# Optimization experiments

Hardware: AMD Instinct MI355X
Metric: run time of the kernel (lower is better)

Reference implementation:

```python
import jax, jax.numpy as jnp
import numpy as np
from jax import lax

TAU = 0.1
TAU_BASE = 0.1
DIR_W = 1.0
N_LEVELS = 3  # labels has N_LEVELS hierarchy cols + 1 direction col
B, D = 4096, 1024


def setup_inputs() -> dict:
    key = jax.random.key(0)
    k1, k2 = jax.random.split(key)
    embeddings = jax.random.normal(k1, (B, D), dtype=jnp.float32)
    labels = jax.random.randint(k2, (B, N_LEVELS + 1), 0, 8, dtype=jnp.int64)
    return {"embeddings": embeddings, "labels": labels}


def _hier_loss(embeddings, labels):
    # F.normalize(dim=1) with eps=1e-12
    norm = jnp.linalg.norm(embeddings, axis=1, keepdims=True)
    z = embeddings / jnp.maximum(norm, 1e-12)
    hier = labels[:, :-1]          # [B, n_levels]
    dirs = labels[:, -1]           # [B]
    n_levels = hier.shape[1]
    b = z.shape[0]
    eye = jnp.eye(b, dtype=bool)

    sim = (z @ z.T) / TAU                                   # [B, B]
    sim = sim - lax.stop_gradient(jnp.max(sim, axis=1, keepdims=True))
    diff_dir = (dirs[:, None] != dirs[None, :])
    sim = sim - DIR_W * diff_dir.astype(sim.dtype)
    sim = jnp.where(eye, -jnp.inf, sim)
    tiny = jnp.finfo(sim.dtype).tiny
    log_prob = sim - jnp.log(jnp.maximum(jnp.exp(sim).sum(axis=1, keepdims=True), tiny))

    same_dir = ~diff_dir
    total = jnp.zeros((), dtype=sim.dtype)
    max_lower = jnp.full((), -jnp.inf, dtype=sim.dtype)
    seen = jnp.zeros((), dtype=jnp.int32)

    for lvl in range(1, n_levels + 1):  # small fixed loop over hierarchy levels
        same_up_to = jnp.all(hier[:, None, :lvl] == hier[None, :, :lvl], axis=2)  # [B, B]
        pos_mask = same_up_to & same_dir & ~eye
        pos_counts = pos_mask.sum(axis=1)                   # [B] int
        valid = pos_counts > 0
        num_valid = valid.sum()
        any_valid = num_valid > 0

        masked_logp = jnp.where(pos_mask, log_prob, 0.0)
        per_row = masked_logp.sum(axis=1) / jnp.maximum(pos_counts, 1).astype(sim.dtype)
        mean_logp_pos = jnp.sum(jnp.where(valid, per_row, 0.0)) / jnp.maximum(num_valid, 1).astype(sim.dtype)
        raw_loss = -(TAU / TAU_BASE) * mean_logp_pos

        # hmce: running max over levels (max_lower is detached)
        level_loss = jnp.maximum(max_lower, raw_loss)
        max_lower = jnp.where(any_valid,
                              lax.stop_gradient(jnp.maximum(max_lower, level_loss)),
                              max_lower)
        penalty = 2.0 ** (1.0 / lvl)  # h_penalty(1/lvl)
        total = total + jnp.where(any_valid, level_loss * penalty, 0.0)
        seen = seen + any_valid.astype(jnp.int32)

    return total / jnp.maximum(seen, 1).astype(total.dtype)


def reference(embeddings, labels):
    return _hier_loss(embeddings, labels)
```

## Files before the change

kernel.cpp:

```cpp
#include <hip/hip_runtime.h>
#include <hip/hip_bf16.h>
#include <stdint.h>

#define NB 4096
#define ND 1024

typedef __attribute__((ext_vector_type(4))) float f32x4;
typedef __attribute__((ext_vector_type(2))) long i64x2;

__global__ __launch_bounds__(256) void prep_kernel(
    const float* __restrict__ emb, const int* __restrict__ labels,
    unsigned char* __restrict__ zq, int* __restrict__ keys)
{
    const int wid = threadIdx.x >> 6, lane = threadIdx.x & 63;
    const int row = blockIdx.x * 4 + wid;
    const float4* src = (const float4*)(emb + (size_t)row * ND) + lane * 4;
    float4 v[4];
    float ss = 0.0f;
    #pragma unroll
    for (int j = 0; j < 4; ++j) {
        v[j] = src[j];
        ss += v[j].x * v[j].x + v[j].y * v[j].y + v[j].z * v[j].z + v[j].w * v[j].w;
    }
    #pragma unroll
    for (int o = 1; o < 64; o <<= 1) ss += __shfl_xor(ss, o);
    const float inv = 1.0f / fmaxf(sqrtf(ss), 1e-12f);

    const float z0 = v[0].x * inv, z1 = v[0].y * inv, z2 = v[0].z * inv, z3 = v[0].w * inv;
    const float z4 = v[1].x * inv, z5 = v[1].y * inv, z6 = v[1].z * inv, z7 = v[1].w * inv;
    const float z8 = v[2].x * inv, z9 = v[2].y * inv, zA = v[2].z * inv, zB = v[2].w * inv;
    const float zC = v[3].x * inv, zD = v[3].y * inv, zE = v[3].z * inv, zF = v[3].w * inv;

    int p0 = 0, p1 = 0, p2 = 0, p3 = 0;
    p0 = __builtin_amdgcn_cvt_pk_fp8_f32(z0, z1, p0, false);
    p0 = __builtin_amdgcn_cvt_pk_fp8_f32(z2, z3, p0, true);
    p1 = __builtin_amdgcn_cvt_pk_fp8_f32(z4, z5, p1, false);
    p1 = __builtin_amdgcn_cvt_pk_fp8_f32(z6, z7, p1, true);
    p2 = __builtin_amdgcn_cvt_pk_fp8_f32(z8, z9, p2, false);
    p2 = __builtin_amdgcn_cvt_pk_fp8_f32(zA, zB, p2, true);
    p3 = __builtin_amdgcn_cvt_pk_fp8_f32(zC, zD, p3, false);
    p3 = __builtin_amdgcn_cvt_pk_fp8_f32(zE, zF, p3, true);

    const int sf  = (row >> 4) * 16 + (lane >> 2);
    const int sel = (lane >> 1) & 1;
    const int c0  = (lane & 1) * 2;
    const int L0  = (row & 15) + 16 * c0;
    unsigned char* d = zq + (size_t)sf * 1024;
    int2 w01; w01.x = p0; w01.y = p1;
    int2 w23; w23.x = p2; w23.y = p3;
    *(int2*)(d + L0 * 16 + sel * 8)        = w01;
    *(int2*)(d + (L0 + 16) * 16 + sel * 8) = w23;

    if (lane == 0) {
        const int* lr = labels + row * 4;
        keys[row] = ((lr[3] & 7) << 24) | ((lr[0] & 7) << 16) |
                    ((lr[1] & 7) << 8)  |  (lr[2] & 7);
    }
}

__global__ __launch_bounds__(256, 2) void simtile_kernel(
    const unsigned char* __restrict__ zq, const int* __restrict__ keys,
    float* __restrict__ partials)
{
    const int b = blockIdx.x;
    const int p = (b & 7) * 66 + (b >> 3);
    int r = (int)((sqrtf(8.0f * p + 1.0f) - 1.0f) * 0.5f);
    while ((r + 1) * (r + 2) / 2 <= p) ++r;
    while (r * (r + 1) / 2 > p) --r;
    const int bi = p - r * (r + 1) / 2;
    const int bj = r;
    const int I0 = bi * 128, J0 = bj * 128;
    const bool offdiag = (bi != bj);
    const bool diag = !offdiag;

    const int tid = threadIdx.x;
    const int lane = tid & 63, w = tid >> 6;
    const int llo = lane & 15, lhi = lane >> 4;
    const int wm = w >> 1, wn = w & 1;

    __shared__ float epiA[2][128][4];
    __shared__ float epiB[2][128][4];
    __shared__ int keyI[128];
    __shared__ int keyJ[128];

    if (tid < 128) {
        keyI[tid] = keys[I0 + tid];
        keyJ[tid] = keys[J0 + tid];
    }

    const unsigned char* aF = zq + (size_t)(bi * 8 + wm * 4) * 16384 + lane * 16;
    const unsigned char* bF = zq + (size_t)(bj * 8 + wn * 4) * 16384 + lane * 16;

    f32x4 acc[4][4];
    #pragma unroll
    for (int m = 0; m < 4; ++m)
        #pragma unroll
        for (int n = 0; n < 4; ++n)
            acc[m][n] = (f32x4){0.f, 0.f, 0.f, 0.f};

    #define LOADF(A, Bf, T)                                                        \
        do {                                                                       \
            _Pragma("unroll")                                                      \
            for (int m = 0; m < 4; ++m)                                            \
                A[m] = *(const i64x2*)(aF + (size_t)(m) * 16384 + (T) * 1024);     \
            _Pragma("unroll")                                                      \
            for (int n = 0; n < 4; ++n)                                            \
                Bf[n] = *(const i64x2*)(bF + (size_t)(n) * 16384 + (T) * 1024);    \
        } while (0)

    #define STEP(A, Bf)                                                            \
        do {                                                                       \
            _Pragma("unroll")                                                      \
            for (int m = 0; m < 4; ++m)                                            \
                _Pragma("unroll")                                                  \
                for (int n = 0; n < 4; ++n) {                                      \
                    acc[m][n] = __builtin_amdgcn_mfma_f32_16x16x32_fp8_fp8(        \
                        A[m][0], Bf[n][0], acc[m][n], 0, 0, 0);                    \
                    acc[m][n] = __builtin_amdgcn_mfma_f32_16x16x32_fp8_fp8(        \
                        A[m][1], Bf[n][1], acc[m][n], 0, 0, 0);                    \
                }                                                                  \
        } while (0)

    {
        i64x2 aC[4], bC[4], aN[4], bN[4];
        LOADF(aC, bC, 0);
        #pragma unroll 1
        for (int t2 = 0; t2 < 8; ++t2) {
            LOADF(aN, bN, 2 * t2 + 1);
            STEP(aC, bC);
            if (t2 < 7) LOADF(aC, bC, 2 * t2 + 2);
            STEP(aN, bN);
        }
    }
    #undef LOADF
    #undef STEP

    __syncthreads();

    int kJ[4], tcol[4];
    #pragma unroll
    for (int n = 0; n < 4; ++n) {
        tcol[n] = wn * 64 + n * 16 + llo;
        kJ[n] = keyJ[tcol[n]];
    }

    float stB[4][4];
    #pragma unroll
    for (int n = 0; n < 4; ++n)
        #pragma unroll
        for (int s = 0; s < 4; ++s) stB[n][s] = 0.0f;

    #pragma unroll
    for (int m = 0; m < 4; ++m) {
        float stA[4][4];
        #pragma unroll
        for (int rr = 0; rr < 4; ++rr)
            #pragma unroll
            for (int s = 0; s < 4; ++s) stA[rr][s] = 0.0f;

        int kI[4], trow[4];
        #pragma unroll
        for (int rr = 0; rr < 4; ++rr) {
            trow[rr] = wm * 64 + m * 16 + lhi * 4 + rr;
            kI[rr] = keyI[trow[rr]];
        }
        #pragma unroll
        for (int n = 0; n < 4; ++n) {
            #pragma unroll
            for (int rr = 0; rr < 4; ++rr) {
                const float v = acc[m][n][rr] * 10.0f;
                const int x = kI[rr] ^ kJ[n];
                const float pen = (x & 0xFF000000) ? 1.0f : 0.0f;
                const float g = __expf(v - 10.0f - pen);
                if (!(diag && trow[rr] == tcol[n])) {
                    stA[rr][0] += g;           stB[n][0] += g;
                    if ((x & 0xFFFF0000) == 0) { stA[rr][1] += v; stB[n][1] += v; }
                    if ((x & 0xFFFFFF00) == 0) { stA[rr][2] += v; stB[n][2] += v; }
                    if (x == 0)                { stA[rr][3] += v; stB[n][3] += v; }
                }
            }
        }
        #pragma unroll
        for (int rr = 0; rr < 4; ++rr)
            #pragma unroll
            for (int s = 0; s < 4; ++s) {
                float vv = stA[rr][s];
                vv += __shfl_xor(vv, 1);
                vv += __shfl_xor(vv, 2);
                vv += __shfl_xor(vv, 4);
                vv += __shfl_xor(vv, 8);
                stA[rr][s] = vv;
            }
        if (llo == 0) {
            #pragma unroll
            for (int rr = 0; rr < 4; ++rr) {
                float4 o; o.x = stA[rr][0]; o.y = stA[rr][1]; o.z = stA[rr][2]; o.w = stA[rr][3];
                *(float4*)&epiA[wn][trow[rr]][0] = o;
            }
        }
    }
    #pragma unroll
    for (int n = 0; n < 4; ++n)
        #pragma unroll
        for (int s = 0; s < 4; ++s) {
            float vv = stB[n][s];
            vv += __shfl_xor(vv, 16);
            vv += __shfl_xor(vv, 32);
            stB[n][s] = vv;
        }
    if (lhi == 0) {
        #pragma unroll
        for (int n = 0; n < 4; ++n) {
            float4 o; o.x = stB[n][0]; o.y = stB[n][1]; o.z = stB[n][2]; o.w = stB[n][3];
            *(float4*)&epiB[wm][tcol[n]][0] = o;
        }
    }
    __syncthreads();

    if (tid < 128) {
        const float4 a0 = *(const float4*)&epiA[0][tid][0];
        const float4 a1 = *(const float4*)&epiA[1][tid][0];
        float4 o; o.x = a0.x + a1.x; o.y = a0.y + a1.y; o.z = a0.z + a1.z; o.w = a0.w + a1.w;
        *(float4*)(partials + ((size_t)bj * NB + I0 + tid) * 4) = o;
        if (offdiag) {
            const float4 b0 = *(const float4*)&epiB[0][tid][0];
            const float4 b1 = *(const float4*)&epiB[1][tid][0];
            float4 q; q.x = b0.x + b1.x; q.y = b0.y + b1.y; q.z = b0.z + b1.z; q.w = b0.w + b1.w;
            *(float4*)(partials + ((size_t)bi * NB + J0 + tid) * 4) = q;
        }
    }
}

__global__ __launch_bounds__(256) void rowreduce_kernel(
    const float* __restrict__ partials, const int* __restrict__ keys,
    float* __restrict__ blocksums)
{
    const int tid = threadIdx.x;
    const int row = blockIdx.x * 256 + tid;
    const int lane = tid & 63, wid = tid >> 6;

    __shared__ int h3[4096];
    __shared__ int h2[512];
    __shared__ int h1[64];

    for (int i = tid; i < 4096; i += 256) h3[i] = 0;
    __syncthreads();
    for (int i = tid; i < 4096; i += 256) {
        const int k = keys[i];
        const int i3 = (((((k >> 24) & 7) * 8 + ((k >> 16) & 7)) * 8 + ((k >> 8) & 7)) * 8) + (k & 7);
        atomicAdd(&h3[i3], 1);
    }
    __syncthreads();
    for (int i = tid; i < 512; i += 256) {
        int s = 0;
        #pragma unroll
        for (int j = 0; j < 8; ++j) s += h3[i * 8 + j];
        h2[i] = s;
    }
    __syncthreads();
    if (tid < 64) {
        int s = 0;
        #pragma unroll
        for (int j = 0; j < 8; ++j) s += h2[tid * 8 + j];
        h1[tid] = s;
    }
    __syncthreads();

    float G = 0.f, T1 = 0.f, T2 = 0.f, T3 = 0.f;
    for (int ct = 0; ct < 32; ++ct) {
        const float4 u = *(const float4*)(partials + ((size_t)ct * NB + row) * 4);
        G += u.x; T1 += u.y; T2 += u.z; T3 += u.w;
    }
    const float lg = logf(fmaxf(G, 1e-30f)) + 10.0f;

    const int key = keys[row];
    const int i1 = ((key >> 24) & 7) * 8 + ((key >> 16) & 7);
    const int i2 = i1 * 8 + ((key >> 8) & 7);
    const int i3 = i2 * 8 + (key & 7);
    const int C[3] = {h1[i1] - 1, h2[i2] - 1, h3[i3] - 1};
    const float T[3] = {T1, T2, T3};

    float vals[6];
    #pragma unroll
    for (int l = 0; l < 3; ++l) {
        const bool valid = C[l] > 0;
        const float pr = T[l] / fmaxf((float)C[l], 1.0f) - lg;
        vals[2 * l]     = valid ? pr : 0.0f;
        vals[2 * l + 1] = valid ? 1.0f : 0.0f;
    }

    __shared__ float red[4][6];
    #pragma unroll
    for (int s = 0; s < 6; ++s) {
        float v = vals[s];
        #pragma unroll
        for (int o = 32; o > 0; o >>= 1) v += __shfl_xor(v, o);
        vals[s] = v;
    }
    if (lane == 0)
        #pragma unroll
        for (int s = 0; s < 6; ++s) red[wid][s] = vals[s];
    __syncthreads();
    if (tid == 0) {
        #pragma unroll
        for (int s = 0; s < 6; ++s)
            blocksums[blockIdx.x * 8 + s] = red[0][s] + red[1][s] + red[2][s] + red[3][s];
    }
}

__global__ void final_kernel(const float* __restrict__ blocksums, float* __restrict__ out)
{
    if (threadIdx.x != 0) return;
    float sums[6] = {0, 0, 0, 0, 0, 0};
    for (int b = 0; b < 16; ++b)
        for (int s = 0; s < 6; ++s) sums[s] += blocksums[b * 8 + s];

    const float pen[3] = {2.0f, 1.41421356237309515f, 1.25992104989487319f};
    float total = 0.0f, max_lower = -INFINITY;
    int seen = 0;
    for (int l = 0; l < 3; ++l) {
        const float nv   = sums[2 * l + 1];
        const bool  any  = nv > 0.0f;
        const float mean = sums[2 * l] / fmaxf(nv, 1.0f);
        const float raw  = -mean;
        const float lvl  = fmaxf(max_lower, raw);
        if (any) {
            total += lvl * pen[l];
            max_lower = fmaxf(max_lower, lvl);
            seen++;
        }
    }
    out[0] = total / (float)(seen > 0 ? seen : 1);
}

extern "C" void kernel_launch(void* const* d_in, const int* in_sizes, int n_in,
                              void* d_out, int out_size, void* d_ws, size_t ws_size,
                              hipStream_t stream)
{
    const float* emb    = (const float*)d_in[0];
    const int*   labels = (const int*)d_in[1];
    float*       out    = (float*)d_out;
    char*        ws     = (char*)d_ws;

    unsigned char* zq    = (unsigned char*)(ws);
    int*   keys     = (int*)(ws + 4194304);
    float* partials = (float*)(ws + 4210688);
    float* bsums    = (float*)(ws + 6307840);

    prep_kernel<<<NB / 4, 256, 0, stream>>>(emb, labels, zq, keys);
    simtile_kernel<<<528, 256, 0, stream>>>(zq, keys, partials);
    rowreduce_kernel<<<NB / 256, 256, 0, stream>>>(partials, keys, bsums);
    final_kernel<<<1, 64, 0, stream>>>(bsums, out);
}
```

Baseline: 49.60 us.

## Stage fp8 prep output in LDS and deepen MFMA load pipeline to three buffers

The prep kernel now handles 16 rows per 1024-thread block. It scatters the fp8-packed normalized rows into a shared-memory tile and then writes the whole 16 KB tile to global memory with coalesced 16-byte stores, replacing the scattered 8-byte global writes. The simtile main loop moves from double-buffered to triple-buffered fragment loads, keeping three K-steps of operands in flight so global load latency is better hidden behind MFMAs. This raises register pressure in a kernel bounded at 2 blocks per CU, and adds a block barrier to the prep kernel.

```diff
diff --git a/kernel.cpp b/kernel.cpp
--- a/kernel.cpp
+++ b/kernel.cpp
@@ -8,12 +8,15 @@
 typedef __attribute__((ext_vector_type(4))) float f32x4;
 typedef __attribute__((ext_vector_type(2))) long i64x2;
 
-__global__ __launch_bounds__(256) void prep_kernel(
+__global__ __launch_bounds__(1024) void prep_kernel(
     const float* __restrict__ emb, const int* __restrict__ labels,
     unsigned char* __restrict__ zq, int* __restrict__ keys)
 {
     const int wid = threadIdx.x >> 6, lane = threadIdx.x & 63;
-    const int row = blockIdx.x * 4 + wid;
+    const int rt  = blockIdx.x;
+    const int row = rt * 16 + wid;
+    __shared__ __align__(16) unsigned char sh[16384];
+
     const float4* src = (const float4*)(emb + (size_t)row * ND) + lane * 4;
     float4 v[4];
     float ss = 0.0f;
@@ -26,26 +29,21 @@
     for (int o = 1; o < 64; o <<= 1) ss += __shfl_xor(ss, o);
     const float inv = 1.0f / fmaxf(sqrtf(ss), 1e-12f);
 
-    const float z0 = v[0].x * inv, z1 = v[0].y * inv, z2 = v[0].z * inv, z3 = v[0].w * inv;
-    const float z4 = v[1].x * inv, z5 = v[1].y * inv, z6 = v[1].z * inv, z7 = v[1].w * inv;
-    const float z8 = v[2].x * inv, z9 = v[2].y * inv, zA = v[2].z * inv, zB = v[2].w * inv;
-    const float zC = v[3].x * inv, zD = v[3].y * inv, zE = v[3].z * inv, zF = v[3].w * inv;
-
     int p0 = 0, p1 = 0, p2 = 0, p3 = 0;
-    p0 = __builtin_amdgcn_cvt_pk_fp8_f32(z0, z1, p0, false);
-    p0 = __builtin_amdgcn_cvt_pk_fp8_f32(z2, z3, p0, true);
-    p1 = __builtin_amdgcn_cvt_pk_fp8_f32(z4, z5, p1, false);
-    p1 = __builtin_amdgcn_cvt_pk_fp8_f32(z6, z7, p1, true);
-    p2 = __builtin_amdgcn_cvt_pk_fp8_f32(z8, z9, p2, false);
-    p2 = __builtin_amdgcn_cvt_pk_fp8_f32(zA, zB, p2, true);
-    p3 = __builtin_amdgcn_cvt_pk_fp8_f32(zC, zD, p3, false);
-    p3 = __builtin_amdgcn_cvt_pk_fp8_f32(zE, zF, p3, true);
-
-    const int sf  = (row >> 4) * 16 + (lane >> 2);
+    p0 = __builtin_amdgcn_cvt_pk_fp8_f32(v[0].x * inv, v[0].y * inv, p0, false);
+    p0 = __builtin_amdgcn_cvt_pk_fp8_f32(v[0].z * inv, v[0].w * inv, p0, true);
+    p1 = __builtin_amdgcn_cvt_pk_fp8_f32(v[1].x * inv, v[1].y * inv, p1, false);
+    p1 = __builtin_amdgcn_cvt_pk_fp8_f32(v[1].z * inv, v[1].w * inv, p1, true);
+    p2 = __builtin_amdgcn_cvt_pk_fp8_f32(v[2].x * inv, v[2].y * inv, p2, false);
+    p2 = __builtin_amdgcn_cvt_pk_fp8_f32(v[2].z * inv, v[2].w * inv, p2, true);
+    p3 = __builtin_amdgcn_cvt_pk_fp8_f32(v[3].x * inv, v[3].y * inv, p3, false);
+    p3 = __builtin_amdgcn_cvt_pk_fp8_f32(v[3].z * inv, v[3].w * inv, p3, true);
+
+    const int sfl = lane >> 2;
     const int sel = (lane >> 1) & 1;
     const int c0  = (lane & 1) * 2;
-    const int L0  = (row & 15) + 16 * c0;
-    unsigned char* d = zq + (size_t)sf * 1024;
+    const int L0  = wid + 16 * c0;
+    unsigned char* d = sh + sfl * 1024;
     int2 w01; w01.x = p0; w01.y = p1;
     int2 w23; w23.x = p2; w23.y = p3;
     *(int2*)(d + L0 * 16 + sel * 8)        = w01;
@@ -56,6 +54,9 @@
         keys[row] = ((lr[3] & 7) << 24) | ((lr[0] & 7) << 16) |
                     ((lr[1] & 7) << 8)  |  (lr[2] & 7);
     }
+    __syncthreads();
+    const int t = threadIdx.x;
+    *(int4*)(zq + (size_t)rt * 16384 + t * 16) = *(const int4*)(sh + t * 16);
 }
 
 __global__ __launch_bounds__(256, 2) void simtile_kernel(
@@ -122,15 +123,20 @@
         } while (0)
 
     {
-        i64x2 aC[4], bC[4], aN[4], bN[4];
-        LOADF(aC, bC, 0);
+        i64x2 a0[4], b0[4], a1[4], b1[4], a2[4], b2[4];
+        LOADF(a0, b0, 0);
+        LOADF(a1, b1, 1);
+        LOADF(a2, b2, 2);
         #pragma unroll 1
-        for (int t2 = 0; t2 < 8; ++t2) {
-            LOADF(aN, bN, 2 * t2 + 1);
-            STEP(aC, bC);
-            if (t2 < 7) LOADF(aC, bC, 2 * t2 + 2);
-            STEP(aN, bN);
-        }
+        for (int t = 0; t < 4; ++t) {
+            STEP(a0, b0); LOADF(a0, b0, 3 * t + 3);
+            STEP(a1, b1); LOADF(a1, b1, 3 * t + 4);
+            STEP(a2, b2); LOADF(a2, b2, 3 * t + 5);
+        }
+        STEP(a0, b0); LOADF(a0, b0, 15);
+        STEP(a1, b1);
+        STEP(a2, b2);
+        STEP(a0, b0);
     }
     #undef LOADF
     #undef STEP
@@ -347,7 +353,7 @@
     float* partials = (float*)(ws + 4210688);
     float* bsums    = (float*)(ws + 6307840);
 
-    prep_kernel<<<NB / 4, 256, 0, stream>>>(emb, labels, zq, keys);
+    prep_kernel<<<NB / 16, 1024, 0, stream>>>(emb, labels, zq, keys);
     simtile_kernel<<<528, 256, 0, stream>>>(zq, keys, partials);
     rowreduce_kernel<<<NB / 256, 256, 0, stream>>>(partials, keys, bsums);
     final_kernel<<<1, 64, 0, stream>>>(bsums, out);
```

New measurement: 53.68 us. +8.2%, slower.

## Shrink similarity tiles to 64x64 single-wave blocks with direct partial writes

Applied to the files above, without the earlier changes.

The symmetric similarity tiling moves from 128x128 tiles computed by four waves to 64x64 tiles computed by one wave. That gives 2080 blocks instead of 528, and the shared-memory epilogue and its block barriers go away because each wave writes its row and column partials straight to global memory. The row-reduce kernel now sums 64 column-tile partials instead of 32, and the workspace offsets are moved to fit the larger partial buffer. The aim is better load balance and occupancy across the CUs. The cost is less operand reuse per tile, more global traffic and more partials to reduce.

```diff
diff --git a/kernel.cpp b/kernel.cpp
--- a/kernel.cpp
+++ b/kernel.cpp
@@ -26,20 +26,15 @@
     for (int o = 1; o < 64; o <<= 1) ss += __shfl_xor(ss, o);
     const float inv = 1.0f / fmaxf(sqrtf(ss), 1e-12f);
 
-    const float z0 = v[0].x * inv, z1 = v[0].y * inv, z2 = v[0].z * inv, z3 = v[0].w * inv;
-    const float z4 = v[1].x * inv, z5 = v[1].y * inv, z6 = v[1].z * inv, z7 = v[1].w * inv;
-    const float z8 = v[2].x * inv, z9 = v[2].y * inv, zA = v[2].z * inv, zB = v[2].w * inv;
-    const float zC = v[3].x * inv, zD = v[3].y * inv, zE = v[3].z * inv, zF = v[3].w * inv;
-
     int p0 = 0, p1 = 0, p2 = 0, p3 = 0;
-    p0 = __builtin_amdgcn_cvt_pk_fp8_f32(z0, z1, p0, false);
-    p0 = __builtin_amdgcn_cvt_pk_fp8_f32(z2, z3, p0, true);
-    p1 = __builtin_amdgcn_cvt_pk_fp8_f32(z4, z5, p1, false);
-    p1 = __builtin_amdgcn_cvt_pk_fp8_f32(z6, z7, p1, true);
-    p2 = __builtin_amdgcn_cvt_pk_fp8_f32(z8, z9, p2, false);
-    p2 = __builtin_amdgcn_cvt_pk_fp8_f32(zA, zB, p2, true);
-    p3 = __builtin_amdgcn_cvt_pk_fp8_f32(zC, zD, p3, false);
-    p3 = __builtin_amdgcn_cvt_pk_fp8_f32(zE, zF, p3, true);
+    p0 = __builtin_amdgcn_cvt_pk_fp8_f32(v[0].x * inv, v[0].y * inv, p0, false);
+    p0 = __builtin_amdgcn_cvt_pk_fp8_f32(v[0].z * inv, v[0].w * inv, p0, true);
+    p1 = __builtin_amdgcn_cvt_pk_fp8_f32(v[1].x * inv, v[1].y * inv, p1, false);
+    p1 = __builtin_amdgcn_cvt_pk_fp8_f32(v[1].z * inv, v[1].w * inv, p1, true);
+    p2 = __builtin_amdgcn_cvt_pk_fp8_f32(v[2].x * inv, v[2].y * inv, p2, false);
+    p2 = __builtin_amdgcn_cvt_pk_fp8_f32(v[2].z * inv, v[2].w * inv, p2, true);
+    p3 = __builtin_amdgcn_cvt_pk_fp8_f32(v[3].x * inv, v[3].y * inv, p3, false);
+    p3 = __builtin_amdgcn_cvt_pk_fp8_f32(v[3].z * inv, v[3].w * inv, p3, true);
 
     const int sf  = (row >> 4) * 16 + (lane >> 2);
     const int sel = (lane >> 1) & 1;
@@ -58,38 +53,32 @@
     }
 }
 
-__global__ __launch_bounds__(256, 2) void simtile_kernel(
+__global__ __launch_bounds__(64, 2) void simtile_kernel(
     const unsigned char* __restrict__ zq, const int* __restrict__ keys,
     float* __restrict__ partials)
 {
     const int b = blockIdx.x;
-    const int p = (b & 7) * 66 + (b >> 3);
+    const int p = (b & 7) * 260 + (b >> 3);
     int r = (int)((sqrtf(8.0f * p + 1.0f) - 1.0f) * 0.5f);
     while ((r + 1) * (r + 2) / 2 <= p) ++r;
     while (r * (r + 1) / 2 > p) --r;
     const int bi = p - r * (r + 1) / 2;
     const int bj = r;
-    const int I0 = bi * 128, J0 = bj * 128;
+    const int I0 = bi * 64, J0 = bj * 64;
     const bool offdiag = (bi != bj);
     const bool diag = !offdiag;
 
-    const int tid = threadIdx.x;
-    const int lane = tid & 63, w = tid >> 6;
+    const int lane = threadIdx.x;
     const int llo = lane & 15, lhi = lane >> 4;
-    const int wm = w >> 1, wn = w & 1;
-
-    __shared__ float epiA[2][128][4];
-    __shared__ float epiB[2][128][4];
-    __shared__ int keyI[128];
-    __shared__ int keyJ[128];
-
-    if (tid < 128) {
-        keyI[tid] = keys[I0 + tid];
-        keyJ[tid] = keys[J0 + tid];
-    }
-
-    const unsigned char* aF = zq + (size_t)(bi * 8 + wm * 4) * 16384 + lane * 16;
-    const unsigned char* bF = zq + (size_t)(bj * 8 + wn * 4) * 16384 + lane * 16;
+
+    __shared__ int keyI[64];
+    __shared__ int keyJ[64];
+    keyI[lane] = keys[I0 + lane];
+    keyJ[lane] = keys[J0 + lane];
+    __syncthreads();
+
+    const unsigned char* aF = zq + (size_t)(bi * 4) * 16384 + lane * 16;
+    const unsigned char* bF = zq + (size_t)(bj * 4) * 16384 + lane * 16;
 
     f32x4 acc[4][4];
     #pragma unroll
@@ -135,12 +124,10 @@
     #undef LOADF
     #undef STEP
 
-    __syncthreads();
-
     int kJ[4], tcol[4];
     #pragma unroll
     for (int n = 0; n < 4; ++n) {
-        tcol[n] = wn * 64 + n * 16 + llo;
+        tcol[n] = n * 16 + llo;
         kJ[n] = keyJ[tcol[n]];
     }
 
@@ -161,7 +148,7 @@
         int kI[4], trow[4];
         #pragma unroll
         for (int rr = 0; rr < 4; ++rr) {
-            trow[rr] = wm * 64 + m * 16 + lhi * 4 + rr;
+            trow[rr] = m * 16 + lhi * 4 + rr;
             kI[rr] = keyI[trow[rr]];
         }
         #pragma unroll
@@ -195,7 +182,7 @@
             #pragma unroll
             for (int rr = 0; rr < 4; ++rr) {
                 float4 o; o.x = stA[rr][0]; o.y = stA[rr][1]; o.z = stA[rr][2]; o.w = stA[rr][3];
-                *(float4*)&epiA[wn][trow[rr]][0] = o;
+                *(float4*)(partials + ((size_t)bj * NB + I0 + trow[rr]) * 4) = o;
             }
         }
     }
@@ -208,25 +195,11 @@
             vv += __shfl_xor(vv, 32);
             stB[n][s] = vv;
         }
-    if (lhi == 0) {
+    if (lhi == 0 && offdiag) {
         #pragma unroll
         for (int n = 0; n < 4; ++n) {
             float4 o; o.x = stB[n][0]; o.y = stB[n][1]; o.z = stB[n][2]; o.w = stB[n][3];
-            *(float4*)&epiB[wm][tcol[n]][0] = o;
-        }
-    }
-    __syncthreads();
-
-    if (tid < 128) {
-        const float4 a0 = *(const float4*)&epiA[0][tid][0];
-        const float4 a1 = *(const float4*)&epiA[1][tid][0];
-        float4 o; o.x = a0.x + a1.x; o.y = a0.y + a1.y; o.z = a0.z + a1.z; o.w = a0.w + a1.w;
-        *(float4*)(partials + ((size_t)bj * NB + I0 + tid) * 4) = o;
-        if (offdiag) {
-            const float4 b0 = *(const float4*)&epiB[0][tid][0];
-            const float4 b1 = *(const float4*)&epiB[1][tid][0];
-            float4 q; q.x = b0.x + b1.x; q.y = b0.y + b1.y; q.z = b0.z + b1.z; q.w = b0.w + b1.w;
-            *(float4*)(partials + ((size_t)bi * NB + J0 + tid) * 4) = q;
+            *(float4*)(partials + ((size_t)bi * NB + J0 + tcol[n]) * 4) = o;
         }
     }
 }
@@ -267,7 +240,7 @@
     __syncthreads();
 
     float G = 0.f, T1 = 0.f, T2 = 0.f, T3 = 0.f;
-    for (int ct = 0; ct < 32; ++ct) {
+    for (int ct = 0; ct < 64; ++ct) {
         const float4 u = *(const float4*)(partials + ((size_t)ct * NB + row) * 4);
         G += u.x; T1 += u.y; T2 += u.z; T3 += u.w;
     }
@@ -345,10 +318,10 @@
     unsigned char* zq    = (unsigned char*)(ws);
     int*   keys     = (int*)(ws + 4194304);
     float* partials = (float*)(ws + 4210688);
-    float* bsums    = (float*)(ws + 6307840);
+    float* bsums    = (float*)(ws + 8404992);
 
     prep_kernel<<<NB / 4, 256, 0, stream>>>(emb, labels, zq, keys);
-    simtile_kernel<<<528, 256, 0, stream>>>(zq, keys, partials);
+    simtile_kernel<<<2080, 64, 0, stream>>>(zq, keys, partials);
     rowreduce_kernel<<<NB / 256, 256, 0, stream>>>(partials, keys, bsums);
     final_kernel<<<1, 64, 0, stream>>>(bsums, out);
 }
```

New measurement: 50.12 us. About the same (+1.1%).
